# Optimization experiments

Hardware: AMD Instinct MI355X
Metric: run time of the kernel (lower is better)

## Reference

```python
import jax, jax.numpy as jnp
import numpy as np

TWO_PI = 6.283185307179586


def setup_inputs() -> dict:
    key = jax.random.key(0)
    k1, k2, k3, k4, k5, k6 = jax.random.split(key, 6)
    B, T, D = 2, 8192, 1024
    x = jax.random.normal(k1, (B, T, D), dtype=jnp.float32)
    # nn.Linear weights are [out, in]; init with small scale like torch default
    s = 1.0 / np.sqrt(D)
    Wk = jax.random.uniform(k2, (D, D), jnp.float32, -s, s)
    Wv = jax.random.uniform(k3, (D, D), jnp.float32, -s, s)
    Wo = jax.random.uniform(k4, (D, D), jnp.float32, -s, s)
    # random phasor frequencies in [0, 2*pi)
    freqs = jax.random.uniform(k5, (D,), jnp.float32, 0.0, TWO_PI)
    return {"x": x, "Wk": Wk, "Wv": Wv, "Wo": Wo, "freqs": freqs}


def reference(x, Wk, Wv, Wo, freqs):
    B, T, C = x.shape
    # k projection is computed in the original forward but never used downstream
    k_real = x @ Wk.T  # [B,T,D] (dead value, kept for fidelity)
    v_real = x @ Wv.T  # [B,T,D]
    v = v_real.astype(jnp.complex64)
    # rotors: per-position unit phasors exp(i * t * freqs), shape [T, D]
    t = jnp.arange(T, dtype=jnp.float32)
    rotors = jnp.exp(1j * (t[:, None] * freqs[None, :])).astype(jnp.complex64)
    # bind each value with its rotor and accumulate causally (O(N) memory trace)
    memory_trace = jnp.cumsum(v * rotors[None, :, :], axis=1)  # [B,T,D] complex64
    # retrieve by unbinding with the conjugate rotor; take the real component
    retrieved = jnp.real(memory_trace * jnp.conj(rotors)[None, :, :])  # [B,T,D]
    return retrieved @ Wo.T
```

## Files before the change

### kernel.cpp

```cpp
#include <hip/hip_runtime.h>
#include <hip/hip_bf16.h>


#define B_  2
#define T_  8192
#define D_  1024
#define BT_ 16384
#define CS_ 64
#define NCHUNK_ 128

typedef __attribute__((ext_vector_type(4))) float f32x4;
typedef __attribute__((ext_vector_type(8))) short bf16x8;

static __device__ inline unsigned short f2bf(float f) {
    union { float f; unsigned int u; } a;
    a.f = f;
    unsigned int u = a.u;
    return (unsigned short)((u + 0x7FFFu + ((u >> 16) & 1u)) >> 16);
}
static __device__ inline float bf2f(unsigned short h) {
    union { unsigned int u; float f; } a;
    a.u = ((unsigned int)h) << 16;
    return a.f;
}

__global__ __launch_bounds__(256) void cast_all(const float* __restrict__ x,
                                                const float* __restrict__ Wv,
                                                const float* __restrict__ Wo,
                                                unsigned short* __restrict__ xb,
                                                unsigned short* __restrict__ wvb,
                                                unsigned short* __restrict__ wob) {
    const int nx = BT_ * D_ / 4;
    const int nw = D_ * D_ / 4;
    int i = blockIdx.x * 256 + threadIdx.x;
    const float4* src;
    unsigned short* dst;
    int j;
    if (i < nx)            { src = (const float4*)x;  dst = xb;  j = i; }
    else if (i < nx + nw)  { src = (const float4*)Wv; dst = wvb; j = i - nx; }
    else                   { src = (const float4*)Wo; dst = wob; j = i - nx - nw; }
    float4 v = src[j];
    ushort4 o;
    o.x = f2bf(v.x); o.y = f2bf(v.y); o.z = f2bf(v.z); o.w = f2bf(v.w);
    ((ushort4*)dst)[j] = o;
}

template <bool BF16OUT, bool FUSE_SUMS>
__global__ __launch_bounds__(256) void gemm_bt(const short* __restrict__ A,
                                               const short* __restrict__ Bm,
                                               void* __restrict__ Cout,
                                               const float* __restrict__ freqs,
                                               float* __restrict__ csum,
                                               int M, int N, int K) {
    __shared__ short lds[16384];
    const int lane = threadIdx.x & 63;
    const int wave = threadIdx.x >> 6;
    const int wr = wave >> 1, wc = wave & 1;

    const int nb = N >> 7;
    const int id = blockIdx.x;
    const int xcd = id & 7;
    const int slot = id >> 3;
    const int bn = (slot % nb) * 128;
    const int bm = (xcd * ((M >> 7) >> 3) + slot / nb) * 128;

    const int sr = lane >> 3;
    const int cb = lane & 7;
    const short* ga[4];
    const short* gb[4];
#pragma unroll
    for (int cc = 0; cc < 4; ++cc) {
        const int chunk = wave * 4 + cc;
        const int row = chunk * 8 + sr;
        const int col = (cb ^ (row & 7)) * 8;
        ga[cc] = A + (size_t)(bm + row) * K + col;
        gb[cc] = Bm + (size_t)(bn + row) * K + col;
    }

    const int c4r = lane >> 4;
    int aoff[4][2], boff[4][2];
#pragma unroll
    for (int i = 0; i < 4; ++i) {
        const int m = wr * 64 + (lane & 15) + i * 16;
        const int n = wc * 64 + (lane & 15) + i * 16;
#pragma unroll
        for (int ks = 0; ks < 2; ++ks) {
            aoff[i][ks] = m * 64 + (((ks * 4 + c4r) ^ (m & 7)) * 8);
            boff[i][ks] = 8192 + n * 64 + (((ks * 4 + c4r) ^ (n & 7)) * 8);
        }
    }

    f32x4 acc[4][4] = {};

    for (int k0 = 0; k0 < K; k0 += 64) {
#pragma unroll
        for (int cc = 0; cc < 4; ++cc) {
            const int chunk = wave * 4 + cc;
            __builtin_amdgcn_global_load_lds(
                (const __attribute__((address_space(1))) void*)(ga[cc] + k0),
                (__attribute__((address_space(3))) void*)&lds[chunk * 512], 16, 0, 0);
            __builtin_amdgcn_global_load_lds(
                (const __attribute__((address_space(1))) void*)(gb[cc] + k0),
                (__attribute__((address_space(3))) void*)&lds[8192 + chunk * 512], 16, 0, 0);
        }
        __syncthreads();
#pragma unroll
        for (int ks = 0; ks < 2; ++ks) {
            bf16x8 a[4], b[4];
#pragma unroll
            for (int i = 0; i < 4; ++i) a[i] = *(const bf16x8*)&lds[aoff[i][ks]];
#pragma unroll
            for (int j = 0; j < 4; ++j) b[j] = *(const bf16x8*)&lds[boff[j][ks]];
#pragma unroll
            for (int i = 0; i < 4; ++i)
#pragma unroll
                for (int j = 0; j < 4; ++j)
                    acc[i][j] = __builtin_amdgcn_mfma_f32_16x16x32_bf16(a[i], b[j], acc[i][j], 0, 0, 0);
        }
        __syncthreads();
    }

    const int row0 = c4r * 4;
#pragma unroll
    for (int i = 0; i < 4; ++i) {
#pragma unroll
        for (int j = 0; j < 4; ++j) {
            const int col = bn + wc * 64 + j * 16 + (lane & 15);
#pragma unroll
            for (int r = 0; r < 4; ++r) {
                const size_t row = bm + wr * 64 + i * 16 + row0 + r;
                if constexpr (BF16OUT)
                    ((unsigned short*)Cout)[row * N + col] = f2bf(acc[i][j][r]);
                else
                    ((float*)Cout)[row * N + col] = acc[i][j][r];
            }
        }
    }

    if constexpr (FUSE_SUMS) {
        const int b = bm >> 13;
        const int trow = bm & 8191;
        const int chunk = (trow >> 6) + wr;
        const int t0 = trow + wr * 64 + c4r * 4;
#pragma unroll
        for (int j = 0; j < 4; ++j) {
            const int d = bn + wc * 64 + j * 16 + (lane & 15);
            const float f = freqs[d];
            float ss, cc2;
            sincosf((float)t0 * f, &ss, &cc2);
            float s1, c1;
            sincosf(f, &s1, &c1);
            float c2 = c1 * c1 - s1 * s1, s2 = 2.f * c1 * s1;
            float c4 = c2 * c2 - s2 * s2, s4 = 2.f * c2 * s2;
            float c8 = c4 * c4 - s4 * s4, s8 = 2.f * c4 * s4;
            float c12 = c8 * c4 - s8 * s4, s12 = s8 * c4 + c8 * s4;
            float c13 = c12 * c1 - s12 * s1, s13 = s12 * c1 + c12 * s1;
            float ar = 0.f, ai = 0.f;
            float cr = cc2, sr2 = ss;
#pragma unroll
            for (int i = 0; i < 4; ++i) {
#pragma unroll
                for (int r = 0; r < 4; ++r) {
                    const float w = acc[i][j][r];
                    ar = fmaf(w, cr, ar); ai = fmaf(w, sr2, ai);
                    const float ec = (r < 3) ? c1 : c13;
                    const float es = (r < 3) ? s1 : s13;
                    const float nc = cr * ec - sr2 * es;
                    const float ns = sr2 * ec + cr * es;
                    cr = nc; sr2 = ns;
                }
            }
            ar += __shfl_xor(ar, 16); ai += __shfl_xor(ai, 16);
            ar += __shfl_xor(ar, 32); ai += __shfl_xor(ai, 32);
            if (c4r == 0)
                *(float2*)(csum + (((size_t)b * NCHUNK_ + chunk) * D_ + d) * 2) =
                    make_float2(ar, ai);
        }
    }
}

__global__ __launch_bounds__(256) void scan_pass2(float* __restrict__ csum) {
    const int g = blockIdx.x * 256 + threadIdx.x;
    const int b = g / D_;
    const int d = g % D_;
    float2* cs = (float2*)csum;
    const size_t base = (size_t)b * NCHUNK_ * D_ + d;
    float pr = 0.f, pi = 0.f;
    for (int cc = 0; cc < NCHUNK_; cc += 32) {
        float2 buf[32];
#pragma unroll
        for (int k = 0; k < 32; ++k) buf[k] = cs[base + (size_t)(cc + k) * D_];
#pragma unroll
        for (int k = 0; k < 32; ++k) {
            float r = buf[k].x, im = buf[k].y;
            buf[k] = make_float2(pr, pi);
            pr += r; pi += im;
        }
#pragma unroll
        for (int k = 0; k < 32; ++k) cs[base + (size_t)(cc + k) * D_] = buf[k];
    }
}

__global__ __launch_bounds__(256) void scan_pass3(const unsigned short* __restrict__ v,
                                                  const float* __restrict__ freqs,
                                                  const float* __restrict__ csum,
                                                  unsigned short* __restrict__ ret) {
    const int chunk = blockIdx.x;
    const int d0 = blockIdx.y * 512 + threadIdx.x * 2;
    const int b = blockIdx.z;

    float fr[2], s[2], c[2], sf[2], cf[2], ar[2], ai[2];
    {
        float2 f2 = *(const float2*)(freqs + d0);
        fr[0] = f2.x; fr[1] = f2.y;
    }
    const float t0f = (float)(chunk * CS_);
#pragma unroll
    for (int k = 0; k < 2; ++k) {
        sincosf(t0f * fr[k], &s[k], &c[k]);
        sincosf(fr[k], &sf[k], &cf[k]);
    }
    {
        const float4 o = *(const float4*)(csum + (((size_t)b * NCHUNK_ + chunk) * D_ + d0) * 2);
        ar[0] = o.x; ai[0] = o.y; ar[1] = o.z; ai[1] = o.w;
    }
    const unsigned int* vp = (const unsigned int*)(v + ((size_t)b * T_ + chunk * CS_) * D_ + d0);
    unsigned int* rp = (unsigned int*)(ret + ((size_t)b * T_ + chunk * CS_) * D_ + d0);
    for (int tb = 0; tb < CS_; tb += 8) {
        unsigned int w[8];
#pragma unroll
        for (int u = 0; u < 8; ++u) w[u] = vp[(size_t)(tb + u) * (D_ / 2)];
#pragma unroll
        for (int u = 0; u < 8; ++u) {
            float wv[2], o[2];
            wv[0] = bf2f((unsigned short)w[u]);
            wv[1] = bf2f((unsigned short)(w[u] >> 16));
#pragma unroll
            for (int k = 0; k < 2; ++k) {
                ar[k] = fmaf(wv[k], c[k], ar[k]);
                ai[k] = fmaf(wv[k], s[k], ai[k]);
                o[k] = ar[k] * c[k] + ai[k] * s[k];
                float nc = c[k] * cf[k] - s[k] * sf[k];
                float ns = s[k] * cf[k] + c[k] * sf[k];
                c[k] = nc; s[k] = ns;
            }
            rp[(size_t)(tb + u) * (D_ / 2)] =
                (unsigned int)f2bf(o[0]) | ((unsigned int)f2bf(o[1]) << 16);
        }
    }
}

extern "C" void kernel_launch(void* const* d_in, const int* in_sizes, int n_in,
                              void* d_out, int out_size, void* d_ws, size_t ws_size,
                              hipStream_t stream) {
    const float* x     = (const float*)d_in[0];
    const float* Wv    = (const float*)d_in[2];
    const float* Wo    = (const float*)d_in[3];
    const float* freqs = (const float*)d_in[4];
    float* out = (float*)d_out;

    char* ws = (char*)d_ws;
    unsigned short* x_bf  = (unsigned short*)ws;
    unsigned short* Wv_bf = (unsigned short*)(ws + 33554432);
    unsigned short* Wo_bf = (unsigned short*)(ws + 35651584);
    unsigned short* ret   = (unsigned short*)(ws + 37748736);
    float*          csum  = (float*)(ws + 71303168);
    unsigned short* v_bf = (unsigned short*)d_out;

    cast_all<<<(BT_ * D_ / 4 + 2 * D_ * D_ / 4) / 256, 256, 0, stream>>>(
        x, Wv, Wo, x_bf, Wv_bf, Wo_bf);

    gemm_bt<true, true><<<(BT_ / 128) * (D_ / 128), 256, 0, stream>>>(
        (const short*)x_bf, (const short*)Wv_bf, (void*)v_bf, freqs, csum, BT_, D_, D_);

    scan_pass2<<<(B_ * D_) / 256, 256, 0, stream>>>(csum);
    dim3 p3grid(NCHUNK_, D_ / 512, B_);
    scan_pass3<<<p3grid, 256, 0, stream>>>(v_bf, freqs, csum, ret);

    gemm_bt<false, false><<<(BT_ / 128) * (D_ / 128), 256, 0, stream>>>(
        (const short*)ret, (const short*)Wo_bf, (void*)out, nullptr, nullptr, BT_, D_, D_);
}
```

Baseline: 240.3 us.

## Drop separate chunk-prefix scan kernel; sum preceding chunk totals in scan pass

Removes the scan_pass2 launch. Each scan_pass3 block now sums the totals of all earlier chunks directly from csum, which costs redundant O(chunk) reads per block but saves one kernel launch and one serial pass. The GEMM templates are also split into two specialized kernels with launch_bounds(256,5) to hint occupancy. The redundant reads total about 128*127/2*16KB, or roughly 130MB, which mostly hit in cache but could add latency for late chunks.

```diff
diff --git a/kernel.cpp b/kernel.cpp
--- a/kernel.cpp
+++ b/kernel.cpp
@@ -45,80 +45,77 @@
     ((ushort4*)dst)[j] = o;
 }
 
-template <bool BF16OUT, bool FUSE_SUMS>
-__global__ __launch_bounds__(256) void gemm_bt(const short* __restrict__ A,
-                                               const short* __restrict__ Bm,
-                                               void* __restrict__ Cout,
-                                               const float* __restrict__ freqs,
-                                               float* __restrict__ csum,
-                                               int M, int N, int K) {
-    __shared__ short lds[16384];
-    const int lane = threadIdx.x & 63;
-    const int wave = threadIdx.x >> 6;
-    const int wr = wave >> 1, wc = wave & 1;
-
-    const int nb = N >> 7;
-    const int id = blockIdx.x;
-    const int xcd = id & 7;
-    const int slot = id >> 3;
-    const int bn = (slot % nb) * 128;
-    const int bm = (xcd * ((M >> 7) >> 3) + slot / nb) * 128;
-
-    const int sr = lane >> 3;
-    const int cb = lane & 7;
-    const short* ga[4];
-    const short* gb[4];
-#pragma unroll
-    for (int cc = 0; cc < 4; ++cc) {
-        const int chunk = wave * 4 + cc;
-        const int row = chunk * 8 + sr;
-        const int col = (cb ^ (row & 7)) * 8;
-        ga[cc] = A + (size_t)(bm + row) * K + col;
-        gb[cc] = Bm + (size_t)(bn + row) * K + col;
-    }
-
-    const int c4r = lane >> 4;
-    int aoff[4][2], boff[4][2];
-#pragma unroll
-    for (int i = 0; i < 4; ++i) {
-        const int m = wr * 64 + (lane & 15) + i * 16;
-        const int n = wc * 64 + (lane & 15) + i * 16;
-#pragma unroll
-        for (int ks = 0; ks < 2; ++ks) {
-            aoff[i][ks] = m * 64 + (((ks * 4 + c4r) ^ (m & 7)) * 8);
-            boff[i][ks] = 8192 + n * 64 + (((ks * 4 + c4r) ^ (n & 7)) * 8);
-        }
-    }
-
-    f32x4 acc[4][4] = {};
-
-    for (int k0 = 0; k0 < K; k0 += 64) {
-#pragma unroll
-        for (int cc = 0; cc < 4; ++cc) {
-            const int chunk = wave * 4 + cc;
-            __builtin_amdgcn_global_load_lds(
-                (const __attribute__((address_space(1))) void*)(ga[cc] + k0),
-                (__attribute__((address_space(3))) void*)&lds[chunk * 512], 16, 0, 0);
-            __builtin_amdgcn_global_load_lds(
-                (const __attribute__((address_space(1))) void*)(gb[cc] + k0),
-                (__attribute__((address_space(3))) void*)&lds[8192 + chunk * 512], 16, 0, 0);
-        }
-        __syncthreads();
-#pragma unroll
-        for (int ks = 0; ks < 2; ++ks) {
-            bf16x8 a[4], b[4];
-#pragma unroll
-            for (int i = 0; i < 4; ++i) a[i] = *(const bf16x8*)&lds[aoff[i][ks]];
-#pragma unroll
-            for (int j = 0; j < 4; ++j) b[j] = *(const bf16x8*)&lds[boff[j][ks]];
-#pragma unroll
-            for (int i = 0; i < 4; ++i)
-#pragma unroll
-                for (int j = 0; j < 4; ++j)
-                    acc[i][j] = __builtin_amdgcn_mfma_f32_16x16x32_bf16(a[i], b[j], acc[i][j], 0, 0, 0);
-        }
-        __syncthreads();
-    }
+#define GEMM_PROLOGUE(A_, B_ptr, M_, N_, K_)                                     \
+    __shared__ short lds[16384];                                                 \
+    const int lane = threadIdx.x & 63;                                           \
+    const int wave = threadIdx.x >> 6;                                           \
+    const int wr = wave >> 1, wc = wave & 1;                                     \
+    const int nb = (N_) >> 7;                                                    \
+    const int id = blockIdx.x;                                                   \
+    const int xcd = id & 7;                                                      \
+    const int slot = id >> 3;                                                    \
+    const int bn = (slot % nb) * 128;                                            \
+    const int bm = (xcd * (((M_) >> 7) >> 3) + slot / nb) * 128;                 \
+    const int sr = lane >> 3;                                                    \
+    const int cb = lane & 7;                                                     \
+    const short* ga[4];                                                          \
+    const short* gb[4];                                                          \
+    _Pragma("unroll")                                                            \
+    for (int cc = 0; cc < 4; ++cc) {                                             \
+        const int chunk = wave * 4 + cc;                                         \
+        const int row = chunk * 8 + sr;                                          \
+        const int col = (cb ^ (row & 7)) * 8;                                    \
+        ga[cc] = (A_) + (size_t)(bm + row) * (K_) + col;                         \
+        gb[cc] = (B_ptr) + (size_t)(bn + row) * (K_) + col;                      \
+    }                                                                            \
+    const int c4r = lane >> 4;                                                   \
+    int aoff[4][2], boff[4][2];                                                  \
+    _Pragma("unroll")                                                            \
+    for (int i = 0; i < 4; ++i) {                                                \
+        const int m = wr * 64 + (lane & 15) + i * 16;                            \
+        const int n = wc * 64 + (lane & 15) + i * 16;                            \
+        _Pragma("unroll")                                                        \
+        for (int ks = 0; ks < 2; ++ks) {                                         \
+            aoff[i][ks] = m * 64 + (((ks * 4 + c4r) ^ (m & 7)) * 8);             \
+            boff[i][ks] = 8192 + n * 64 + (((ks * 4 + c4r) ^ (n & 7)) * 8);      \
+        }                                                                        \
+    }                                                                            \
+    f32x4 acc[4][4] = {};                                                        \
+    for (int k0 = 0; k0 < (K_); k0 += 64) {                                      \
+        _Pragma("unroll")                                                        \
+        for (int cc = 0; cc < 4; ++cc) {                                         \
+            const int chunk = wave * 4 + cc;                                     \
+            __builtin_amdgcn_global_load_lds(                                    \
+                (const __attribute__((address_space(1))) void*)(ga[cc] + k0),    \
+                (__attribute__((address_space(3))) void*)&lds[chunk * 512], 16, 0, 0); \
+            __builtin_amdgcn_global_load_lds(                                    \
+                (const __attribute__((address_space(1))) void*)(gb[cc] + k0),    \
+                (__attribute__((address_space(3))) void*)&lds[8192 + chunk * 512], 16, 0, 0); \
+        }                                                                        \
+        __syncthreads();                                                         \
+        _Pragma("unroll")                                                        \
+        for (int ks = 0; ks < 2; ++ks) {                                         \
+            bf16x8 a[4], b[4];                                                   \
+            _Pragma("unroll")                                                    \
+            for (int i = 0; i < 4; ++i) a[i] = *(const bf16x8*)&lds[aoff[i][ks]];\
+            _Pragma("unroll")                                                    \
+            for (int j = 0; j < 4; ++j) b[j] = *(const bf16x8*)&lds[boff[j][ks]];\
+            _Pragma("unroll")                                                    \
+            for (int i = 0; i < 4; ++i)                                          \
+                _Pragma("unroll")                                                \
+                for (int j = 0; j < 4; ++j)                                      \
+                    acc[i][j] = __builtin_amdgcn_mfma_f32_16x16x32_bf16(         \
+                        a[i], b[j], acc[i][j], 0, 0, 0);                         \
+        }                                                                        \
+        __syncthreads();                                                         \
+    }
+
+__global__ __launch_bounds__(256, 5) void gemm1_fused(const short* __restrict__ A,
+                                                      const short* __restrict__ Bm,
+                                                      unsigned short* __restrict__ Cout,
+                                                      const float* __restrict__ freqs,
+                                                      float* __restrict__ csum) {
+    GEMM_PROLOGUE(A, Bm, BT_, D_, D_)
 
     const int row0 = c4r * 4;
 #pragma unroll
@@ -129,75 +126,68 @@
 #pragma unroll
             for (int r = 0; r < 4; ++r) {
                 const size_t row = bm + wr * 64 + i * 16 + row0 + r;
-                if constexpr (BF16OUT)
-                    ((unsigned short*)Cout)[row * N + col] = f2bf(acc[i][j][r]);
-                else
-                    ((float*)Cout)[row * N + col] = acc[i][j][r];
-            }
-        }
-    }
-
-    if constexpr (FUSE_SUMS) {
-        const int b = bm >> 13;
-        const int trow = bm & 8191;
-        const int chunk = (trow >> 6) + wr;
-        const int t0 = trow + wr * 64 + c4r * 4;
+                Cout[row * D_ + col] = f2bf(acc[i][j][r]);
+            }
+        }
+    }
+
+    const int b = bm >> 13;
+    const int trow = bm & 8191;
+    const int chunk = (trow >> 6) + wr;
+    const int t0 = trow + wr * 64 + c4r * 4;
+#pragma unroll
+    for (int j = 0; j < 4; ++j) {
+        const int d = bn + wc * 64 + j * 16 + (lane & 15);
+        const float f = freqs[d];
+        float ss, cc2;
+        sincosf((float)t0 * f, &ss, &cc2);
+        float s1, c1;
+        sincosf(f, &s1, &c1);
+        float c2 = c1 * c1 - s1 * s1, s2 = 2.f * c1 * s1;
+        float c4 = c2 * c2 - s2 * s2, s4 = 2.f * c2 * s2;
+        float c8 = c4 * c4 - s4 * s4, s8 = 2.f * c4 * s4;
+        float c12 = c8 * c4 - s8 * s4, s12 = s8 * c4 + c8 * s4;
+        float c13 = c12 * c1 - s12 * s1, s13 = s12 * c1 + c12 * s1;
+        float ar = 0.f, ai = 0.f;
+        float cr = cc2, sr2 = ss;
+#pragma unroll
+        for (int i = 0; i < 4; ++i) {
+#pragma unroll
+            for (int r = 0; r < 4; ++r) {
+                const float w = acc[i][j][r];
+                ar = fmaf(w, cr, ar); ai = fmaf(w, sr2, ai);
+                const float ec = (r < 3) ? c1 : c13;
+                const float es = (r < 3) ? s1 : s13;
+                const float nc = cr * ec - sr2 * es;
+                const float ns = sr2 * ec + cr * es;
+                cr = nc; sr2 = ns;
+            }
+        }
+        ar += __shfl_xor(ar, 16); ai += __shfl_xor(ai, 16);
+        ar += __shfl_xor(ar, 32); ai += __shfl_xor(ai, 32);
+        if (c4r == 0)
+            *(float2*)(csum + (((size_t)b * NCHUNK_ + chunk) * D_ + d) * 2) =
+                make_float2(ar, ai);
+    }
+}
+
+__global__ __launch_bounds__(256, 5) void gemm2_plain(const short* __restrict__ A,
+                                                      const short* __restrict__ Bm,
+                                                      float* __restrict__ Cout) {
+    GEMM_PROLOGUE(A, Bm, BT_, D_, D_)
+
+    const int row0 = c4r * 4;
+#pragma unroll
+    for (int i = 0; i < 4; ++i) {
 #pragma unroll
         for (int j = 0; j < 4; ++j) {
-            const int d = bn + wc * 64 + j * 16 + (lane & 15);
-            const float f = freqs[d];
-            float ss, cc2;
-            sincosf((float)t0 * f, &ss, &cc2);
-            float s1, c1;
-            sincosf(f, &s1, &c1);
-            float c2 = c1 * c1 - s1 * s1, s2 = 2.f * c1 * s1;
-            float c4 = c2 * c2 - s2 * s2, s4 = 2.f * c2 * s2;
-            float c8 = c4 * c4 - s4 * s4, s8 = 2.f * c4 * s4;
-            float c12 = c8 * c4 - s8 * s4, s12 = s8 * c4 + c8 * s4;
-            float c13 = c12 * c1 - s12 * s1, s13 = s12 * c1 + c12 * s1;
-            float ar = 0.f, ai = 0.f;
-            float cr = cc2, sr2 = ss;
-#pragma unroll
-            for (int i = 0; i < 4; ++i) {
-#pragma unroll
-                for (int r = 0; r < 4; ++r) {
-                    const float w = acc[i][j][r];
-                    ar = fmaf(w, cr, ar); ai = fmaf(w, sr2, ai);
-                    const float ec = (r < 3) ? c1 : c13;
-                    const float es = (r < 3) ? s1 : s13;
-                    const float nc = cr * ec - sr2 * es;
-                    const float ns = sr2 * ec + cr * es;
-                    cr = nc; sr2 = ns;
-                }
-            }
-            ar += __shfl_xor(ar, 16); ai += __shfl_xor(ai, 16);
-            ar += __shfl_xor(ar, 32); ai += __shfl_xor(ai, 32);
-            if (c4r == 0)
-                *(float2*)(csum + (((size_t)b * NCHUNK_ + chunk) * D_ + d) * 2) =
-                    make_float2(ar, ai);
-        }
-    }
-}
-
-__global__ __launch_bounds__(256) void scan_pass2(float* __restrict__ csum) {
-    const int g = blockIdx.x * 256 + threadIdx.x;
-    const int b = g / D_;
-    const int d = g % D_;
-    float2* cs = (float2*)csum;
-    const size_t base = (size_t)b * NCHUNK_ * D_ + d;
-    float pr = 0.f, pi = 0.f;
-    for (int cc = 0; cc < NCHUNK_; cc += 32) {
-        float2 buf[32];
-#pragma unroll
-        for (int k = 0; k < 32; ++k) buf[k] = cs[base + (size_t)(cc + k) * D_];
-#pragma unroll
-        for (int k = 0; k < 32; ++k) {
-            float r = buf[k].x, im = buf[k].y;
-            buf[k] = make_float2(pr, pi);
-            pr += r; pi += im;
-        }
-#pragma unroll
-        for (int k = 0; k < 32; ++k) cs[base + (size_t)(cc + k) * D_] = buf[k];
+            const int col = bn + wc * 64 + j * 16 + (lane & 15);
+#pragma unroll
+            for (int r = 0; r < 4; ++r) {
+                const size_t row = bm + wr * 64 + i * 16 + row0 + r;
+                Cout[row * D_ + col] = acc[i][j][r];
+            }
+        }
     }
 }
 
@@ -209,7 +199,28 @@
     const int d0 = blockIdx.y * 512 + threadIdx.x * 2;
     const int b = blockIdx.z;
 
-    float fr[2], s[2], c[2], sf[2], cf[2], ar[2], ai[2];
+    float ar[2] = {0.f, 0.f}, ai[2] = {0.f, 0.f};
+    {
+        const float* cbase = csum + ((size_t)b * NCHUNK_ * D_ + d0) * 2;
+        int cc = 0;
+        for (; cc + 8 <= chunk; cc += 8) {
+            float4 o[8];
+#pragma unroll
+            for (int u = 0; u < 8; ++u)
+                o[u] = *(const float4*)(cbase + (size_t)(cc + u) * (D_ * 2));
+#pragma unroll
+            for (int u = 0; u < 8; ++u) {
+                ar[0] += o[u].x; ai[0] += o[u].y;
+                ar[1] += o[u].z; ai[1] += o[u].w;
+            }
+        }
+        for (; cc < chunk; ++cc) {
+            float4 o = *(const float4*)(cbase + (size_t)cc * (D_ * 2));
+            ar[0] += o.x; ai[0] += o.y; ar[1] += o.z; ai[1] += o.w;
+        }
+    }
+
+    float fr[2], s[2], c[2], sf[2], cf[2];
     {
         float2 f2 = *(const float2*)(freqs + d0);
         fr[0] = f2.x; fr[1] = f2.y;
@@ -219,10 +230,6 @@
     for (int k = 0; k < 2; ++k) {
         sincosf(t0f * fr[k], &s[k], &c[k]);
         sincosf(fr[k], &sf[k], &cf[k]);
-    }
-    {
-        const float4 o = *(const float4*)(csum + (((size_t)b * NCHUNK_ + chunk) * D_ + d0) * 2);
-        ar[0] = o.x; ai[0] = o.y; ar[1] = o.z; ai[1] = o.w;
     }
     const unsigned int* vp = (const unsigned int*)(v + ((size_t)b * T_ + chunk * CS_) * D_ + d0);
     unsigned int* rp = (unsigned int*)(ret + ((size_t)b * T_ + chunk * CS_) * D_ + d0);
@@ -270,13 +277,12 @@
     cast_all<<<(BT_ * D_ / 4 + 2 * D_ * D_ / 4) / 256, 256, 0, stream>>>(
         x, Wv, Wo, x_bf, Wv_bf, Wo_bf);
 
-    gemm_bt<true, true><<<(BT_ / 128) * (D_ / 128), 256, 0, stream>>>(
-        (const short*)x_bf, (const short*)Wv_bf, (void*)v_bf, freqs, csum, BT_, D_, D_);
-
-    scan_pass2<<<(B_ * D_) / 256, 256, 0, stream>>>(csum);
+    gemm1_fused<<<(BT_ / 128) * (D_ / 128), 256, 0, stream>>>(
+        (const short*)x_bf, (const short*)Wv_bf, v_bf, freqs, csum);
+
     dim3 p3grid(NCHUNK_, D_ / 512, B_);
     scan_pass3<<<p3grid, 256, 0, stream>>>(v_bf, freqs, csum, ret);
 
-    gemm_bt<false, false><<<(BT_ / 128) * (D_ / 128), 256, 0, stream>>>(
-        (const short*)ret, (const short*)Wo_bf, (void*)out, nullptr, nullptr, BT_, D_, D_);
-}
+    gemm2_plain<<<(BT_ / 128) * (D_ / 128), 256, 0, stream>>>(
+        (const short*)ret, (const short*)Wo_bf, out);
+}
```

New measurement: 447.0 us. 1.86x slower.
